# Kernel tuning notes

Measured on AMD Instinct MI355X. Metric: run time of the kernel, lower is better.

Reference implementation:

```python
import jax, jax.numpy as jnp
import numpy as np

B, S, D, H, DK = 2, 2048, 1024, 16, 64  # d_model = n_heads * d_k

def setup_inputs() -> dict:
    key = jax.random.key(0)
    ks = jax.random.split(key, 11)
    s = 1.0 / np.sqrt(D)
    return {
        "Q": jax.random.normal(ks[0], (B, S, D), jnp.float32),
        "K": jax.random.normal(ks[1], (B, S, D), jnp.float32),
        "V": jax.random.normal(ks[2], (B, S, D), jnp.float32),
        "wq": jax.random.normal(ks[3], (D, D), jnp.float32) * s,
        "bq": jnp.zeros((D,), jnp.float32),
        "wk": jax.random.normal(ks[4], (D, D), jnp.float32) * s,
        "bk": jnp.zeros((D,), jnp.float32),
        "wv": jax.random.normal(ks[5], (D, D), jnp.float32) * s,
        "bv": jnp.zeros((D,), jnp.float32),
        "wo": jax.random.normal(ks[6], (D, D), jnp.float32) * s,
        "bo": jnp.zeros((D,), jnp.float32),
    }

def reference(Q, K, V, wq, bq, wk, bk, wv, bv, wo, bo):
    # linear projections (torch Linear: x @ W^T + b)
    q = Q @ wq.T + bq
    k = K @ wk.T + bk
    v = V @ wv.T + bv
    # split heads -> [B, H, S, DK]
    def split(t):
        return t.reshape(B, S, H, DK).transpose(0, 2, 1, 3)
    q, k, v = split(q), split(k), split(v)
    scale = 1.0 / np.sqrt(DK)
    scores = jnp.einsum('bhqd,bhkd->bhqk', q, k) * scale  # [B,H,S,S]
    probs = jax.nn.softmax(scores, axis=-1)
    # dropout is identity in eval mode
    ctx = jnp.einsum('bhqk,bhkd->bhqd', probs, v)  # [B,H,S,DK]
    ctx = ctx.transpose(0, 2, 1, 3).reshape(B, S, D)
    return ctx @ wo.T + bo
```

## Files before the change

kernel.cpp:

```cpp
#include <hip/hip_runtime.h>

#define S_LEN 2048
#define DMODEL 1024
#define DHEAD 64

typedef _Float16 half8 __attribute__((ext_vector_type(8)));
typedef _Float16 half4 __attribute__((ext_vector_type(4)));
typedef float f32x4 __attribute__((ext_vector_type(4)));
typedef int i32x2 __attribute__((ext_vector_type(2)));

#define LOG2E 1.4426950408889634f

__device__ __forceinline__ void async_copy16(const void* g, void* l) {
  __builtin_amdgcn_global_load_lds((__attribute__((address_space(1))) const void*)g,
                                   (__attribute__((address_space(3))) void*)l,
                                   16, 0, 0);
}

__device__ __forceinline__ void stage16_cvt(const float* __restrict__ gp, _Float16* lp) {
  float4 f0 = ((const float4*)gp)[0];
  float4 f1 = ((const float4*)gp)[1];
  float4 f2 = ((const float4*)gp)[2];
  float4 f3 = ((const float4*)gp)[3];
  half8 h0, h1;
  h0[0] = (_Float16)f0.x; h0[1] = (_Float16)f0.y; h0[2] = (_Float16)f0.z; h0[3] = (_Float16)f0.w;
  h0[4] = (_Float16)f1.x; h0[5] = (_Float16)f1.y; h0[6] = (_Float16)f1.z; h0[7] = (_Float16)f1.w;
  h1[0] = (_Float16)f2.x; h1[1] = (_Float16)f2.y; h1[2] = (_Float16)f2.z; h1[3] = (_Float16)f2.w;
  h1[4] = (_Float16)f3.x; h1[5] = (_Float16)f3.y; h1[6] = (_Float16)f3.z; h1[7] = (_Float16)f3.w;
  *(half8*)lp = h0;
  *(half8*)(lp + 8) = h1;
}

__global__ __launch_bounds__(256) void convert_w(const float* __restrict__ wq,
                                                 const float* __restrict__ wk,
                                                 const float* __restrict__ wv,
                                                 _Float16* __restrict__ dst) {
  const float* src = (blockIdx.y == 0) ? wq : (blockIdx.y == 1) ? wk : wv;
  _Float16* d = dst + (size_t)blockIdx.y * (DMODEL * DMODEL);
  int i = (blockIdx.x * 256 + threadIdx.x) * 4;
  float4 v = *(const float4*)(src + i);
  half4 h;
  h[0] = (_Float16)v.x; h[1] = (_Float16)v.y;
  h[2] = (_Float16)v.z; h[3] = (_Float16)v.w;
  *(half4*)(d + i) = h;
}

__global__ __launch_bounds__(256) void convert_wo(const float* __restrict__ wo,
                                                  _Float16* __restrict__ dst) {
  int i = (blockIdx.x * 256 + threadIdx.x) * 4;
  float4 v = *(const float4*)(wo + i);
  half4 h;
  h[0] = (_Float16)v.x; h[1] = (_Float16)v.y;
  h[2] = (_Float16)v.z; h[3] = (_Float16)v.w;
  *(half4*)(dst + i) = h;
}

__global__ __launch_bounds__(256) void qkv_gemm(
    const float* __restrict__ Qf, const float* __restrict__ Kf, const float* __restrict__ Vf,
    const _Float16* __restrict__ wh,
    const float* __restrict__ bq, const float* __restrict__ bk, const float* __restrict__ bv,
    _Float16* __restrict__ qo, _Float16* __restrict__ ko, _Float16* __restrict__ vt) {
  __shared__ __align__(16) _Float16 As[128 * 32];
  __shared__ __align__(16) _Float16 Bs[128 * 32];
  const int tid = threadIdx.x;
  const int wave = tid >> 6, lane = tid & 63;
  const int m15 = lane & 15, quad = lane >> 4;
  const int m0 = blockIdx.x * 128;
  const int gn0 = blockIdx.y * 128;
  const int sel = gn0 >> 10;
  const int n0 = gn0 & 1023;
  const float* Ag = (sel == 0) ? Qf : (sel == 1) ? Kf : Vf;
  const _Float16* Wg = wh + (size_t)sel * (DMODEL * DMODEL);
  const float* bias = (sel == 0) ? bq : (sel == 1) ? bk : bv;

  const int wm = (wave & 1) * 64, wn = (wave >> 1) * 64;
  const int sr = tid >> 1, sc16 = (tid & 1) * 16;

  f32x4 acc[4][4];
#pragma unroll
  for (int i = 0; i < 4; i++)
#pragma unroll
    for (int j = 0; j < 4; j++) {
      f32x4 z = {0.f, 0.f, 0.f, 0.f};
      acc[i][j] = z;
    }

  for (int k0 = 0; k0 < DMODEL; k0 += 32) {
#pragma unroll
    for (int p = 0; p < 2; p++) {
      int e = p * 2048 + tid * 8;
      async_copy16(Wg + (size_t)(n0 + (e >> 5)) * DMODEL + k0 + (e & 31),
                   (char*)Bs + p * 4096 + wave * 1024);
    }
    stage16_cvt(Ag + (size_t)(m0 + sr) * DMODEL + k0 + sc16, &As[sr * 32 + sc16]);
    __syncthreads();
    half8 af[4], bf[4];
#pragma unroll
    for (int i = 0; i < 4; i++)
      af[i] = *(const half8*)&As[(wm + i * 16 + m15) * 32 + quad * 8];
#pragma unroll
    for (int j = 0; j < 4; j++)
      bf[j] = *(const half8*)&Bs[(wn + j * 16 + m15) * 32 + quad * 8];
#pragma unroll
    for (int i = 0; i < 4; i++)
#pragma unroll
      for (int j = 0; j < 4; j++)
        acc[i][j] = __builtin_amdgcn_mfma_f32_16x16x32_f16(af[i], bf[j], acc[i][j], 0, 0, 0);
    __syncthreads();
  }
  if (sel != 2) {
    _Float16* outp = (sel == 0) ? qo : ko;
    const float scale = (sel == 0) ? (0.125f * LOG2E) : 1.0f;
#pragma unroll
    for (int i = 0; i < 4; i++) {
#pragma unroll
      for (int j = 0; j < 4; j++) {
        int gn = n0 + wn + j * 16 + m15;
        float bb = bias[gn];
#pragma unroll
        for (int r = 0; r < 4; r++) {
          int gm = m0 + wm + i * 16 + quad * 4 + r;
          outp[(size_t)gm * DMODEL + gn] = (_Float16)((acc[i][j][r] + bb) * scale);
        }
      }
    }
  } else {
#pragma unroll
    for (int i = 0; i < 4; i++) {
      int gm0 = m0 + wm + i * 16 + quad * 4;
      int b = gm0 >> 11, s = gm0 & 2047;
#pragma unroll
      for (int j = 0; j < 4; j++) {
        int gn = n0 + wn + j * 16 + m15;
        int h = gn >> 6, dk = gn & 63;
        float bb = bias[gn];
        half4 hv;
        hv[0] = (_Float16)(acc[i][j][0] + bb);
        hv[1] = (_Float16)(acc[i][j][1] + bb);
        hv[2] = (_Float16)(acc[i][j][2] + bb);
        hv[3] = (_Float16)(acc[i][j][3] + bb);
        *(half4*)(vt + ((size_t)(b * 16 + h) * 64 + dk) * 2048 + s) = hv;
      }
    }
  }
}

__global__ __launch_bounds__(256) void attn_kernel(const _Float16* __restrict__ qh,
                                                   const _Float16* __restrict__ kh,
                                                   const _Float16* __restrict__ vt,
                                                   _Float16* __restrict__ ctx) {
  __shared__ __align__(16) char smem[32768];
  const int tid = threadIdx.x;
  const int wave = tid >> 6, lane = tid & 63;
  const int m15 = lane & 15, qd = lane >> 4;
  const int q0 = blockIdx.x * 64;
  const int h = blockIdx.y, b = blockIdx.z;
  const size_t base = (size_t)b * S_LEN * DMODEL + (size_t)h * DHEAD;
  const size_t vbase = (size_t)(b * 16 + h) * 64 * 2048;

  half8 qf[4][2];
#pragma unroll
  for (int qt = 0; qt < 4; qt++) {
    const _Float16* qp = qh + base + (size_t)(q0 + qt * 16 + m15) * DMODEL + qd * 8;
    qf[qt][0] = *(const half8*)qp;
    qf[qt][1] = *(const half8*)(qp + 32);
  }

  const int l8 = lane >> 3, s8 = lane & 7;
  const int swz = (s8 ^ l8) * 8;
  const _Float16* ksrc = kh + base + (size_t)(wave * 8 + l8) * DMODEL + swz;
  const _Float16* vsrc = vt + vbase + (size_t)(wave * 8 + l8) * S_LEN + swz;
  char* kdst = smem + wave * 1024;
  char* vdst = smem + 16384 + wave * 1024;

  const int kcol0 = ((qd ^ (m15 & 7)) << 4);
  const int vcol = ((((wave * 2 + (qd >> 1)) ^ (m15 & 7)) << 4) + (qd & 1) * 8);

  f32x4 acc[4][4];
#pragma unroll
  for (int i = 0; i < 4; i++)
#pragma unroll
    for (int j = 0; j < 4; j++) { f32x4 z = {0.f, 0.f, 0.f, 0.f}; acc[i][j] = z; }
  float ls[4] = {0.f, 0.f, 0.f, 0.f};

#pragma unroll
  for (int p = 0; p < 2; p++) {
    async_copy16(ksrc + (size_t)(p * 32) * DMODEL, kdst + p * 4096);
    async_copy16(vsrc + (size_t)(p * 32) * S_LEN, vdst + p * 4096);
  }
  __syncthreads();

  for (int it = 0; it < 32; it++) {
    const int buf = it & 1;
    if (it < 31) {
      const int kv = (it + 1) * 64;
#pragma unroll
      for (int p = 0; p < 2; p++) {
        async_copy16(ksrc + (size_t)(kv + p * 32) * DMODEL, kdst + (buf ^ 1) * 8192 + p * 4096);
        async_copy16(vsrc + (size_t)(p * 32) * S_LEN + kv, vdst + (buf ^ 1) * 8192 + p * 4096);
      }
    }
    const char* kb = smem + buf * 8192;
    const char* vb = smem + 16384 + buf * 8192;

    half8 kf0 = *(const half8*)(kb + (wave * 16 + m15) * 128 + kcol0);
    half8 kf1 = *(const half8*)(kb + (wave * 16 + m15) * 128 + (kcol0 ^ 64));

    f32x4 sc[4];
#pragma unroll
    for (int qt = 0; qt < 4; qt++) {
      f32x4 z = {0.f, 0.f, 0.f, 0.f};
      sc[qt] = __builtin_amdgcn_mfma_f32_16x16x32_f16(kf0, qf[qt][0], z, 0, 0, 0);
      sc[qt] = __builtin_amdgcn_mfma_f32_16x16x32_f16(kf1, qf[qt][1], sc[qt], 0, 0, 0);
    }

    half4 p[4];
#pragma unroll
    for (int qt = 0; qt < 4; qt++) {
      float e0 = __builtin_amdgcn_exp2f(sc[qt][0]);
      float e1 = __builtin_amdgcn_exp2f(sc[qt][1]);
      float e2 = __builtin_amdgcn_exp2f(sc[qt][2]);
      float e3 = __builtin_amdgcn_exp2f(sc[qt][3]);
      ls[qt] += (e0 + e1) + (e2 + e3);
      i32x2 w2;
      w2[0] = __builtin_bit_cast(int, __builtin_amdgcn_cvt_pkrtz(e0, e1));
      w2[1] = __builtin_bit_cast(int, __builtin_amdgcn_cvt_pkrtz(e2, e3));
      p[qt] = __builtin_bit_cast(half4, w2);
    }

#pragma unroll
    for (int td = 0; td < 4; td++) {
      half4 vf = *(const half4*)(vb + (td * 16 + m15) * 128 + vcol);
#pragma unroll
      for (int qt = 0; qt < 4; qt++)
        acc[td][qt] = __builtin_amdgcn_mfma_f32_16x16x16f16(vf, p[qt], acc[td][qt], 0, 0, 0);
    }
    __syncthreads();
  }

  float* Ored = (float*)smem;
  float* Lred = (float*)(smem + 17408);

#pragma unroll
  for (int qt = 0; qt < 4; qt++) {
    ls[qt] += __shfl_xor(ls[qt], 16);
    ls[qt] += __shfl_xor(ls[qt], 32);
  }
  if (qd == 0) {
#pragma unroll
    for (int qt = 0; qt < 4; qt++) Lred[wave * 64 + qt * 16 + m15] = ls[qt];
  }

  for (int w = 0; w < 4; w++) {
    if (wave == w) {
#pragma unroll
      for (int td = 0; td < 4; td++)
#pragma unroll
        for (int qt = 0; qt < 4; qt++)
#pragma unroll
          for (int r = 0; r < 4; r++) {
            int addr = (qt * 16 + m15) * 65 + td * 16 + qd * 4 + r;
            if (w == 0) Ored[addr] = acc[td][qt][r];
            else        Ored[addr] += acc[td][qt][r];
          }
    }
    __syncthreads();
  }

  {
    const int q = wave * 16 + (lane >> 2);
    const int dc = (lane & 3) * 16;
    const float inv = 1.0f / (Lred[q] + Lred[64 + q] + Lred[128 + q] + Lred[192 + q]);
    const float* rp = Ored + q * 65 + dc;
    half8 h0, h1;
#pragma unroll
    for (int j = 0; j < 8; j++) h0[j] = (_Float16)(rp[j] * inv);
#pragma unroll
    for (int j = 0; j < 8; j++) h1[j] = (_Float16)(rp[8 + j] * inv);
    _Float16* op = ctx + base + (size_t)(q0 + q) * DMODEL + dc;
    *(half8*)op = h0;
    *(half8*)(op + 8) = h1;
  }
}

__global__ __launch_bounds__(256) void out_gemm(const _Float16* __restrict__ ch,
                                                const _Float16* __restrict__ who,
                                                const float* __restrict__ bo,
                                                float* __restrict__ out) {
  __shared__ __align__(16) _Float16 As[128 * 32];
  __shared__ __align__(16) _Float16 Bs[128 * 32];
  const int tid = threadIdx.x;
  const int wave = tid >> 6, lane = tid & 63;
  const int m15 = lane & 15, quad = lane >> 4;
  const int m0 = blockIdx.x * 128, n0 = blockIdx.y * 128;
  const int wm = (wave & 1) * 64, wn = (wave >> 1) * 64;

  f32x4 acc[4][4];
#pragma unroll
  for (int i = 0; i < 4; i++)
#pragma unroll
    for (int j = 0; j < 4; j++) {
      f32x4 z = {0.f, 0.f, 0.f, 0.f};
      acc[i][j] = z;
    }

  for (int k0 = 0; k0 < DMODEL; k0 += 32) {
#pragma unroll
    for (int p = 0; p < 2; p++) {
      int e = p * 2048 + tid * 8;
      async_copy16(ch + (size_t)(m0 + (e >> 5)) * DMODEL + k0 + (e & 31),
                   (char*)As + p * 4096 + wave * 1024);
      async_copy16(who + (size_t)(n0 + (e >> 5)) * DMODEL + k0 + (e & 31),
                   (char*)Bs + p * 4096 + wave * 1024);
    }
    __syncthreads();
    half8 af[4], bf[4];
#pragma unroll
    for (int i = 0; i < 4; i++)
      af[i] = *(const half8*)&As[(wm + i * 16 + m15) * 32 + quad * 8];
#pragma unroll
    for (int j = 0; j < 4; j++)
      bf[j] = *(const half8*)&Bs[(wn + j * 16 + m15) * 32 + quad * 8];
#pragma unroll
    for (int i = 0; i < 4; i++)
#pragma unroll
      for (int j = 0; j < 4; j++)
        acc[i][j] = __builtin_amdgcn_mfma_f32_16x16x32_f16(af[i], bf[j], acc[i][j], 0, 0, 0);
    __syncthreads();
  }
#pragma unroll
  for (int i = 0; i < 4; i++) {
#pragma unroll
    for (int j = 0; j < 4; j++) {
      int gn = n0 + wn + j * 16 + m15;
      float bb = bo[gn];
#pragma unroll
      for (int r = 0; r < 4; r++) {
        int gm = m0 + wm + i * 16 + quad * 4 + r;
        out[(size_t)gm * DMODEL + gn] = acc[i][j][r] + bb;
      }
    }
  }
}

extern "C" void kernel_launch(void* const* d_in, const int* in_sizes, int n_in,
                              void* d_out, int out_size, void* d_ws, size_t ws_size,
                              hipStream_t stream) {
  (void)in_sizes; (void)n_in; (void)out_size; (void)ws_size;
  const float* Q  = (const float*)d_in[0];
  const float* K  = (const float*)d_in[1];
  const float* V  = (const float*)d_in[2];
  const float* wq = (const float*)d_in[3];
  const float* bq = (const float*)d_in[4];
  const float* wk = (const float*)d_in[5];
  const float* bk = (const float*)d_in[6];
  const float* wv = (const float*)d_in[7];
  const float* bv = (const float*)d_in[8];
  const float* wo = (const float*)d_in[9];
  const float* bo = (const float*)d_in[10];
  float* out = (float*)d_out;

  _Float16* qh = (_Float16*)d_out;
  _Float16* kh = qh + (size_t)4194304;
  _Float16* vt = (_Float16*)d_ws;
  _Float16* wh = vt + (size_t)4194304;
  _Float16* ch = vt + (size_t)4194304;
  _Float16* who = (_Float16*)d_ws;

  convert_w<<<dim3(1024, 3), 256, 0, stream>>>(wq, wk, wv, wh);
  qkv_gemm<<<dim3(32, 24), 256, 0, stream>>>(Q, K, V, wh, bq, bk, bv, qh, kh, vt);
  attn_kernel<<<dim3(32, 16, 2), 256, 0, stream>>>(qh, kh, vt, ch);
  convert_wo<<<dim3(1024), 256, 0, stream>>>(wo, who);
  out_gemm<<<dim3(32, 8), 256, 0, stream>>>(ch, who, bo, out);
}
```

Baseline: 261.1 us.

## Split attention waves 2x2 over queries and keys, use 16x16x32 MFMA for PV

Reorganizes the attention work split. The four waves now form a 2x2 grid over query halves and key-tile halves instead of each wave covering all 64 queries for a 16-key slice. The P fragments are rearranged with permlane32/permlane16 swaps so the PV product can use the 16x16x32 MFMA with half8 V loads, which halves the number of PV MFMA issues. The final reduction only merges two waves per query, through one shared-memory pass with a single barrier instead of a four-step serialized accumulate. This adds cross-lane permute instructions and relies on the permute layout being correct.

```diff
diff --git a/kernel.cpp b/kernel.cpp
--- a/kernel.cpp
+++ b/kernel.cpp
@@ -7,7 +7,7 @@
 typedef _Float16 half8 __attribute__((ext_vector_type(8)));
 typedef _Float16 half4 __attribute__((ext_vector_type(4)));
 typedef float f32x4 __attribute__((ext_vector_type(4)));
-typedef int i32x2 __attribute__((ext_vector_type(2)));
+typedef int i32x4 __attribute__((ext_vector_type(4)));
 
 #define LOG2E 1.4426950408889634f
 
@@ -153,15 +153,16 @@
   const int tid = threadIdx.x;
   const int wave = tid >> 6, lane = tid & 63;
   const int m15 = lane & 15, qd = lane >> 4;
+  const int wq = wave >> 1, ws = wave & 1;
   const int q0 = blockIdx.x * 64;
   const int h = blockIdx.y, b = blockIdx.z;
   const size_t base = (size_t)b * S_LEN * DMODEL + (size_t)h * DHEAD;
   const size_t vbase = (size_t)(b * 16 + h) * 64 * 2048;
 
-  half8 qf[4][2];
-#pragma unroll
-  for (int qt = 0; qt < 4; qt++) {
-    const _Float16* qp = qh + base + (size_t)(q0 + qt * 16 + m15) * DMODEL + qd * 8;
+  half8 qf[2][2];
+#pragma unroll
+  for (int qt = 0; qt < 2; qt++) {
+    const _Float16* qp = qh + base + (size_t)(q0 + wq * 32 + qt * 16 + m15) * DMODEL + qd * 8;
     qf[qt][0] = *(const half8*)qp;
     qf[qt][1] = *(const half8*)(qp + 32);
   }
@@ -173,15 +174,16 @@
   char* kdst = smem + wave * 1024;
   char* vdst = smem + 16384 + wave * 1024;
 
-  const int kcol0 = ((qd ^ (m15 & 7)) << 4);
-  const int vcol = ((((wave * 2 + (qd >> 1)) ^ (m15 & 7)) << 4) + (qd & 1) * 8);
-
-  f32x4 acc[4][4];
+  const int kgr = ((qd ^ (m15 & 7)) << 4);
+  const int vgr = (((ws * 4 + qd) ^ (m15 & 7)) << 4);
+  const int krow = ws * 32 + m15;
+
+  f32x4 acc[4][2];
 #pragma unroll
   for (int i = 0; i < 4; i++)
 #pragma unroll
-    for (int j = 0; j < 4; j++) { f32x4 z = {0.f, 0.f, 0.f, 0.f}; acc[i][j] = z; }
-  float ls[4] = {0.f, 0.f, 0.f, 0.f};
+    for (int j = 0; j < 2; j++) { f32x4 z = {0.f, 0.f, 0.f, 0.f}; acc[i][j] = z; }
+  float ls[2] = {0.f, 0.f};
 
 #pragma unroll
   for (int p = 0; p < 2; p++) {
@@ -203,37 +205,57 @@
     const char* kb = smem + buf * 8192;
     const char* vb = smem + 16384 + buf * 8192;
 
-    half8 kf0 = *(const half8*)(kb + (wave * 16 + m15) * 128 + kcol0);
-    half8 kf1 = *(const half8*)(kb + (wave * 16 + m15) * 128 + (kcol0 ^ 64));
-
-    f32x4 sc[4];
-#pragma unroll
-    for (int qt = 0; qt < 4; qt++) {
-      f32x4 z = {0.f, 0.f, 0.f, 0.f};
-      sc[qt] = __builtin_amdgcn_mfma_f32_16x16x32_f16(kf0, qf[qt][0], z, 0, 0, 0);
-      sc[qt] = __builtin_amdgcn_mfma_f32_16x16x32_f16(kf1, qf[qt][1], sc[qt], 0, 0, 0);
-    }
-
-    half4 p[4];
-#pragma unroll
-    for (int qt = 0; qt < 4; qt++) {
-      float e0 = __builtin_amdgcn_exp2f(sc[qt][0]);
-      float e1 = __builtin_amdgcn_exp2f(sc[qt][1]);
-      float e2 = __builtin_amdgcn_exp2f(sc[qt][2]);
-      float e3 = __builtin_amdgcn_exp2f(sc[qt][3]);
-      ls[qt] += (e0 + e1) + (e2 + e3);
-      i32x2 w2;
-      w2[0] = __builtin_bit_cast(int, __builtin_amdgcn_cvt_pkrtz(e0, e1));
-      w2[1] = __builtin_bit_cast(int, __builtin_amdgcn_cvt_pkrtz(e2, e3));
-      p[qt] = __builtin_bit_cast(half4, w2);
+    half8 kf[2][2];
+#pragma unroll
+    for (int t = 0; t < 2; t++) {
+      kf[t][0] = *(const half8*)(kb + (krow + 16 * t) * 128 + kgr);
+      kf[t][1] = *(const half8*)(kb + (krow + 16 * t) * 128 + (kgr ^ 64));
+    }
+
+    f32x4 sc[2][2];
+#pragma unroll
+    for (int t = 0; t < 2; t++)
+#pragma unroll
+      for (int qt = 0; qt < 2; qt++) {
+        f32x4 z = {0.f, 0.f, 0.f, 0.f};
+        sc[t][qt] = __builtin_amdgcn_mfma_f32_16x16x32_f16(kf[t][0], qf[qt][0], z, 0, 0, 0);
+        sc[t][qt] = __builtin_amdgcn_mfma_f32_16x16x32_f16(kf[t][1], qf[qt][1], sc[t][qt], 0, 0, 0);
+      }
+
+    int pk[2][2][2];
+#pragma unroll
+    for (int t = 0; t < 2; t++)
+#pragma unroll
+      for (int qt = 0; qt < 2; qt++) {
+        float e0 = __builtin_amdgcn_exp2f(sc[t][qt][0]);
+        float e1 = __builtin_amdgcn_exp2f(sc[t][qt][1]);
+        float e2 = __builtin_amdgcn_exp2f(sc[t][qt][2]);
+        float e3 = __builtin_amdgcn_exp2f(sc[t][qt][3]);
+        ls[qt] += (e0 + e1) + (e2 + e3);
+        pk[t][qt][0] = __builtin_bit_cast(int, __builtin_amdgcn_cvt_pkrtz(e0, e1));
+        pk[t][qt][1] = __builtin_bit_cast(int, __builtin_amdgcn_cvt_pkrtz(e2, e3));
+      }
+
+    half8 pA[2];
+#pragma unroll
+    for (int qt = 0; qt < 2; qt++) {
+      i32x4 fh;
+#pragma unroll
+      for (int p = 0; p < 2; p++) {
+        auto s1 = __builtin_amdgcn_permlane32_swap(pk[0][qt][p], pk[1][qt][p], false, false);
+        auto s2 = __builtin_amdgcn_permlane16_swap(s1[0], s1[1], false, false);
+        fh[p] = (int)s2[0];
+        fh[2 + p] = (int)s2[1];
+      }
+      pA[qt] = __builtin_bit_cast(half8, fh);
     }
 
 #pragma unroll
     for (int td = 0; td < 4; td++) {
-      half4 vf = *(const half4*)(vb + (td * 16 + m15) * 128 + vcol);
-#pragma unroll
-      for (int qt = 0; qt < 4; qt++)
-        acc[td][qt] = __builtin_amdgcn_mfma_f32_16x16x16f16(vf, p[qt], acc[td][qt], 0, 0, 0);
+      half8 vf = *(const half8*)(vb + (td * 16 + m15) * 128 + vgr);
+#pragma unroll
+      for (int qt = 0; qt < 2; qt++)
+        acc[td][qt] = __builtin_amdgcn_mfma_f32_16x16x32_f16(vf, pA[qt], acc[td][qt], 0, 0, 0);
     }
     __syncthreads();
   }
@@ -242,44 +264,37 @@
   float* Lred = (float*)(smem + 17408);
 
 #pragma unroll
-  for (int qt = 0; qt < 4; qt++) {
+  for (int qt = 0; qt < 2; qt++) {
     ls[qt] += __shfl_xor(ls[qt], 16);
     ls[qt] += __shfl_xor(ls[qt], 32);
   }
-  if (qd == 0) {
-#pragma unroll
-    for (int qt = 0; qt < 4; qt++) Lred[wave * 64 + qt * 16 + m15] = ls[qt];
-  }
-
-  for (int w = 0; w < 4; w++) {
-    if (wave == w) {
+
+  if (ws == 1) {
+#pragma unroll
+    for (int qt = 0; qt < 2; qt++) {
+      int q = wq * 32 + qt * 16 + m15;
+      if (qd == 0) Lred[q] = ls[qt];
 #pragma unroll
       for (int td = 0; td < 4; td++)
-#pragma unroll
-        for (int qt = 0; qt < 4; qt++)
-#pragma unroll
-          for (int r = 0; r < 4; r++) {
-            int addr = (qt * 16 + m15) * 65 + td * 16 + qd * 4 + r;
-            if (w == 0) Ored[addr] = acc[td][qt][r];
-            else        Ored[addr] += acc[td][qt][r];
-          }
-    }
-    __syncthreads();
-  }
-
-  {
-    const int q = wave * 16 + (lane >> 2);
-    const int dc = (lane & 3) * 16;
-    const float inv = 1.0f / (Lred[q] + Lred[64 + q] + Lred[128 + q] + Lred[192 + q]);
-    const float* rp = Ored + q * 65 + dc;
-    half8 h0, h1;
-#pragma unroll
-    for (int j = 0; j < 8; j++) h0[j] = (_Float16)(rp[j] * inv);
-#pragma unroll
-    for (int j = 0; j < 8; j++) h1[j] = (_Float16)(rp[8 + j] * inv);
-    _Float16* op = ctx + base + (size_t)(q0 + q) * DMODEL + dc;
-    *(half8*)op = h0;
-    *(half8*)(op + 8) = h1;
+        *(f32x4*)&Ored[q * 68 + td * 16 + qd * 4] = acc[td][qt];
+    }
+  }
+  __syncthreads();
+
+  if (ws == 0) {
+#pragma unroll
+    for (int qt = 0; qt < 2; qt++) {
+      int q = wq * 32 + qt * 16 + m15;
+      const float inv = 1.0f / (ls[qt] + Lred[q]);
+#pragma unroll
+      for (int td = 0; td < 4; td++) {
+        f32x4 o = acc[td][qt] + *(const f32x4*)&Ored[q * 68 + td * 16 + qd * 4];
+        half4 hv;
+#pragma unroll
+        for (int r = 0; r < 4; r++) hv[r] = (_Float16)(o[r] * inv);
+        *(half4*)(ctx + base + (size_t)(q0 + q) * DMODEL + td * 16 + qd * 4) = hv;
+      }
+    }
   }
 }
 
```

Measured after the change: 248.4 us. 4.9% less time.
